# Optimization experiments

Hardware: AMD Instinct MI355X
Metric: run time of the kernel (lower is better)

Reference implementation:

```python
import jax, jax.numpy as jnp
import numpy as np

TWO_PI = 2.0 * np.pi
ROTATION_PROB = 0.5


def _rodrigues(axis, angle):
    """Vectorized Rodrigues formula. axis: [G,3] (unnormalized), angle: [G] in [0,1) (scaled by 2pi).
    Returns R: [G,3,3]."""
    ax = axis / jnp.linalg.norm(axis, axis=-1, keepdims=True)
    a0, a1, a2 = ax[:, 0], ax[:, 1], ax[:, 2]
    z = jnp.zeros_like(a0)
    # Skew-symmetric cross-product matrix K per graph: [G,3,3]
    K = jnp.stack([
        jnp.stack([z, -a2, a1], axis=-1),
        jnp.stack([a2, z, -a0], axis=-1),
        jnp.stack([-a1, a0, z], axis=-1),
    ], axis=-2)
    theta = (angle * TWO_PI)[:, None, None]
    I = jnp.eye(3, dtype=axis.dtype)
    return I + jnp.sin(theta) * K + (1.0 - jnp.cos(theta)) * jnp.matmul(K, K)


def setup_inputs() -> dict:
    key = jax.random.key(0)
    ks = jax.random.split(key, 8)
    G, N, E = 8192, 2_000_000, 16_000_000
    x = jax.random.normal(ks[0], (N, 3), dtype=jnp.float32)
    edge_attr = jax.random.normal(ks[1], (E, 3), dtype=jnp.float32)
    y = jax.random.normal(ks[2], (G, 3), dtype=jnp.float32)
    node_batch = jnp.sort(jax.random.randint(ks[3], (N,), 0, G, dtype=jnp.int32))
    edge_batch = jnp.sort(jax.random.randint(ks[4], (E,), 0, G, dtype=jnp.int32))
    axis = jax.random.normal(ks[5], (G, 3), dtype=jnp.float32)
    angle = jax.random.uniform(ks[6], (G,), dtype=jnp.float32)
    apply_rand = jax.random.uniform(ks[7], (G,), dtype=jnp.float32)
    return {"x": x, "edge_attr": edge_attr, "y": y, "node_batch": node_batch,
            "edge_batch": edge_batch, "axis": axis, "angle": angle,
            "apply_rand": apply_rand}


def reference(x, edge_attr, y, node_batch, edge_batch, axis, angle, apply_rand):
    R = _rodrigues(axis, angle)  # [G,3,3]
    I = jnp.eye(3, dtype=x.dtype)
    # Only rotate graphs where the coin flip succeeds (identity otherwise)
    R = jnp.where((apply_rand < ROTATION_PROB)[:, None, None], R, I)
    # v @ R.T  ==  out[n,j] = sum_i v[n,i] * R[j,i]
    x_out = jnp.einsum('ni,nji->nj', x, R[node_batch])
    e_out = jnp.einsum('ei,eji->ej', edge_attr, R[edge_batch])
    y_out = jnp.einsum('gi,gji->gj', y, R)
    return x_out, e_out, y_out
```

## Files before the change

### kernel.cpp

```cpp
#include <hip/hip_runtime.h>
#include <math.h>

#define TWO_PI_F 6.283185307179586f
#define ROWS 1024
#define BLK  256

typedef float f32x4 __attribute__((ext_vector_type(4)));

__global__ void compute_R_kernel(const float* __restrict__ axis,
                                 const float* __restrict__ angle,
                                 const float* __restrict__ apply_rand,
                                 float* __restrict__ R, int G) {
    int g = blockIdx.x * blockDim.x + threadIdx.x;
    if (g >= G) return;
    float a = axis[3 * g + 0];
    float b = axis[3 * g + 1];
    float c = axis[3 * g + 2];
    float inv = rsqrtf(a * a + b * b + c * c);
    a *= inv; b *= inv; c *= inv;
    float th = angle[g] * TWO_PI_F;
    float s, co;
    sincosf(th, &s, &co);
    float omc = 1.0f - co;

    float r00 = 1.0f - omc * (b * b + c * c);
    float r01 = -s * c + omc * (a * b);
    float r02 =  s * b + omc * (a * c);
    float r10 =  s * c + omc * (a * b);
    float r11 = 1.0f - omc * (a * a + c * c);
    float r12 = -s * a + omc * (b * c);
    float r20 = -s * b + omc * (a * c);
    float r21 =  s * a + omc * (b * c);
    float r22 = 1.0f - omc * (a * a + b * b);

    if (!(apply_rand[g] < 0.5f)) {
        r00 = 1.0f; r01 = 0.0f; r02 = 0.0f;
        r10 = 0.0f; r11 = 1.0f; r12 = 0.0f;
        r20 = 0.0f; r21 = 0.0f; r22 = 1.0f;
    }
    float4* Rg = reinterpret_cast<float4*>(R + 12 * (size_t)g);
    Rg[0] = make_float4(r00, r01, r02, 0.0f);
    Rg[1] = make_float4(r10, r11, r12, 0.0f);
    Rg[2] = make_float4(r20, r21, r22, 0.0f);
}

template <bool HAS_BATCH>
__global__ __launch_bounds__(BLK) void apply_rot_lds(
        const float* __restrict__ v,
        const int* __restrict__ batch,
        const float* __restrict__ R,
        float* __restrict__ out, int n) {
    __shared__ float buf[ROWS * 3];
    float4* buf4 = reinterpret_cast<float4*>(buf);

    const int tid = threadIdx.x;
    const size_t rowBase = (size_t)blockIdx.x * ROWS;
    int rows = n - (int)rowBase;
    if (rows > ROWS) rows = ROWS;
    const int floatsHere = rows * 3;
    const int f4Here = floatsHere >> 2;
    const int tailFloats = floatsHere & 3;
    const int nRow4 = rows >> 2;

    int4 bi = make_int4(0, 0, 0, 0);
    if (tid < nRow4) {
        if (HAS_BATCH) {
            bi = *(reinterpret_cast<const int4*>(batch + rowBase) + tid);
        } else {
            int base = (int)rowBase + 4 * tid;
            bi = make_int4(base, base + 1, base + 2, base + 3);
        }
    }

    {
        const float4* src = reinterpret_cast<const float4*>(v + rowBase * 3);
        if (tid < f4Here)       buf4[tid]       = src[tid];
        if (tid + 256 < f4Here) buf4[tid + 256] = src[tid + 256];
        if (tid + 512 < f4Here) buf4[tid + 512] = src[tid + 512];
        if (tailFloats && tid < tailFloats) {
            int fi = (f4Here << 2) + tid;
            buf[fi] = v[rowBase * 3 + fi];
        }
    }
    __syncthreads();

    if (tid < nRow4) {
        float4 p0 = buf4[3 * tid + 0];
        float4 p1 = buf4[3 * tid + 1];
        float4 p2 = buf4[3 * tid + 2];
        float rowsv[4][3] = {
            {p0.x, p0.y, p0.z},
            {p0.w, p1.x, p1.y},
            {p1.z, p1.w, p2.x},
            {p2.y, p2.z, p2.w}};
        int gs[4] = {bi.x, bi.y, bi.z, bi.w};
        float oo[12];
#pragma unroll
        for (int r = 0; r < 4; ++r) {
            const float4* Rg = reinterpret_cast<const float4*>(R + 12 * (size_t)gs[r]);
            float4 R0 = Rg[0];
            float4 R1 = Rg[1];
            float4 R2 = Rg[2];
            float v0 = rowsv[r][0], v1 = rowsv[r][1], v2 = rowsv[r][2];
            oo[3 * r + 0] = R0.x * v0 + R0.y * v1 + R0.z * v2;
            oo[3 * r + 1] = R1.x * v0 + R1.y * v1 + R1.z * v2;
            oo[3 * r + 2] = R2.x * v0 + R2.y * v1 + R2.z * v2;
        }
        buf4[3 * tid + 0] = make_float4(oo[0], oo[1], oo[2], oo[3]);
        buf4[3 * tid + 1] = make_float4(oo[4], oo[5], oo[6], oo[7]);
        buf4[3 * tid + 2] = make_float4(oo[8], oo[9], oo[10], oo[11]);
    } else if (tid == nRow4 && (rows & 3)) {
        for (int r = nRow4 * 4; r < rows; ++r) {
            size_t row = rowBase + r;
            int g = HAS_BATCH ? batch[row] : (int)row;
            const float* Rg = R + 12 * (size_t)g;
            float v0 = buf[3 * r + 0], v1 = buf[3 * r + 1], v2 = buf[3 * r + 2];
            float t0 = Rg[0] * v0 + Rg[1] * v1 + Rg[2]  * v2;
            float t1 = Rg[4] * v0 + Rg[5] * v1 + Rg[6]  * v2;
            float t2 = Rg[8] * v0 + Rg[9] * v1 + Rg[10] * v2;
            buf[3 * r + 0] = t0; buf[3 * r + 1] = t1; buf[3 * r + 2] = t2;
        }
    }
    __syncthreads();

    {
        const f32x4* b4 = reinterpret_cast<const f32x4*>(buf);
        f32x4* dst = reinterpret_cast<f32x4*>(out + rowBase * 3);
        if (tid < f4Here) {
            f32x4 val = b4[tid];
            __builtin_nontemporal_store(val, &dst[tid]);
        }
        if (tid + 256 < f4Here) {
            f32x4 val = b4[tid + 256];
            __builtin_nontemporal_store(val, &dst[tid + 256]);
        }
        if (tid + 512 < f4Here) {
            f32x4 val = b4[tid + 512];
            __builtin_nontemporal_store(val, &dst[tid + 512]);
        }
        if (tailFloats && tid < tailFloats) {
            int fi = (f4Here << 2) + tid;
            __builtin_nontemporal_store(buf[fi], &out[rowBase * 3 + fi]);
        }
    }
}

extern "C" void kernel_launch(void* const* d_in, const int* in_sizes, int n_in,
                              void* d_out, int out_size, void* d_ws, size_t ws_size,
                              hipStream_t stream) {
    const float* x          = (const float*)d_in[0];
    const float* edge_attr  = (const float*)d_in[1];
    const float* y          = (const float*)d_in[2];
    const int*   node_batch = (const int*)d_in[3];
    const int*   edge_batch = (const int*)d_in[4];
    const float* axis       = (const float*)d_in[5];
    const float* angle      = (const float*)d_in[6];
    const float* apply_rand = (const float*)d_in[7];

    const int N = in_sizes[3];
    const int E = in_sizes[4];
    const int G = in_sizes[6];

    float* R = (float*)d_ws;
    float* x_out = (float*)d_out;
    float* e_out = x_out + 3 * (size_t)N;
    float* y_out = e_out + 3 * (size_t)E;

    compute_R_kernel<<<(G + BLK - 1) / BLK, BLK, 0, stream>>>(
        axis, angle, apply_rand, R, G);

    int nbN = (N + ROWS - 1) / ROWS;
    int nbE = (E + ROWS - 1) / ROWS;
    int nbG = (G + ROWS - 1) / ROWS;

    apply_rot_lds<true><<<nbE, BLK, 0, stream>>>(edge_attr, edge_batch, R, e_out, E);
    apply_rot_lds<true><<<nbN, BLK, 0, stream>>>(x, node_batch, R, x_out, N);
    apply_rot_lds<false><<<nbG, BLK, 0, stream>>>(y, nullptr, R, y_out, G);
}
```

Baseline: 102.3 us.

## Process two tiles per block with register prefetch of the second tile

Each block now handles two 1024-row tiles. Both tiles' input and batch loads are issued up front into registers. The first tile is then rotated and stored while the second tile's data is still arriving, so more global loads are in flight per thread. This doubles LDS use per block (24 KB) and raises register pressure, which can lower occupancy, and it adds extra barriers.

```diff
diff --git a/kernel.cpp b/kernel.cpp
--- a/kernel.cpp
+++ b/kernel.cpp
@@ -45,45 +45,12 @@
 }
 
 template <bool HAS_BATCH>
-__global__ __launch_bounds__(BLK) void apply_rot_lds(
-        const float* __restrict__ v,
-        const int* __restrict__ batch,
-        const float* __restrict__ R,
-        float* __restrict__ out, int n) {
-    __shared__ float buf[ROWS * 3];
-    float4* buf4 = reinterpret_cast<float4*>(buf);
-
-    const int tid = threadIdx.x;
-    const size_t rowBase = (size_t)blockIdx.x * ROWS;
-    int rows = n - (int)rowBase;
-    if (rows > ROWS) rows = ROWS;
-    const int floatsHere = rows * 3;
-    const int f4Here = floatsHere >> 2;
-    const int tailFloats = floatsHere & 3;
+__device__ __forceinline__ void rotate_tile(float* bufLds, int4 bi,
+                                            const float* __restrict__ R,
+                                            const int* __restrict__ batch,
+                                            size_t rowBase, int rows, int tid) {
+    float4* buf4 = reinterpret_cast<float4*>(bufLds);
     const int nRow4 = rows >> 2;
-
-    int4 bi = make_int4(0, 0, 0, 0);
-    if (tid < nRow4) {
-        if (HAS_BATCH) {
-            bi = *(reinterpret_cast<const int4*>(batch + rowBase) + tid);
-        } else {
-            int base = (int)rowBase + 4 * tid;
-            bi = make_int4(base, base + 1, base + 2, base + 3);
-        }
-    }
-
-    {
-        const float4* src = reinterpret_cast<const float4*>(v + rowBase * 3);
-        if (tid < f4Here)       buf4[tid]       = src[tid];
-        if (tid + 256 < f4Here) buf4[tid + 256] = src[tid + 256];
-        if (tid + 512 < f4Here) buf4[tid + 512] = src[tid + 512];
-        if (tailFloats && tid < tailFloats) {
-            int fi = (f4Here << 2) + tid;
-            buf[fi] = v[rowBase * 3 + fi];
-        }
-    }
-    __syncthreads();
-
     if (tid < nRow4) {
         float4 p0 = buf4[3 * tid + 0];
         float4 p1 = buf4[3 * tid + 1];
@@ -114,34 +81,116 @@
             size_t row = rowBase + r;
             int g = HAS_BATCH ? batch[row] : (int)row;
             const float* Rg = R + 12 * (size_t)g;
-            float v0 = buf[3 * r + 0], v1 = buf[3 * r + 1], v2 = buf[3 * r + 2];
+            float v0 = bufLds[3 * r + 0], v1 = bufLds[3 * r + 1], v2 = bufLds[3 * r + 2];
             float t0 = Rg[0] * v0 + Rg[1] * v1 + Rg[2]  * v2;
             float t1 = Rg[4] * v0 + Rg[5] * v1 + Rg[6]  * v2;
             float t2 = Rg[8] * v0 + Rg[9] * v1 + Rg[10] * v2;
-            buf[3 * r + 0] = t0; buf[3 * r + 1] = t1; buf[3 * r + 2] = t2;
+            bufLds[3 * r + 0] = t0; bufLds[3 * r + 1] = t1; bufLds[3 * r + 2] = t2;
         }
     }
+}
+
+__device__ __forceinline__ void store_tile_nt(const float* bufLds,
+                                              float* __restrict__ out,
+                                              size_t rowBase, int rows, int tid) {
+    const int floatsHere = rows * 3;
+    const int f4Here = floatsHere >> 2;
+    const int tailFloats = floatsHere & 3;
+    const f32x4* b4 = reinterpret_cast<const f32x4*>(bufLds);
+    f32x4* dst = reinterpret_cast<f32x4*>(out + rowBase * 3);
+    if (tid < f4Here) {
+        f32x4 val = b4[tid];
+        __builtin_nontemporal_store(val, &dst[tid]);
+    }
+    if (tid + 256 < f4Here) {
+        f32x4 val = b4[tid + 256];
+        __builtin_nontemporal_store(val, &dst[tid + 256]);
+    }
+    if (tid + 512 < f4Here) {
+        f32x4 val = b4[tid + 512];
+        __builtin_nontemporal_store(val, &dst[tid + 512]);
+    }
+    if (tailFloats && tid < tailFloats) {
+        int fi = (f4Here << 2) + tid;
+        __builtin_nontemporal_store(bufLds[fi], &out[rowBase * 3 + fi]);
+    }
+}
+
+template <bool HAS_BATCH>
+__global__ __launch_bounds__(BLK) void apply_rot_lds2(
+        const float* __restrict__ v,
+        const int* __restrict__ batch,
+        const float* __restrict__ R,
+        float* __restrict__ out, int n) {
+    __shared__ float buf[2][ROWS * 3];
+    const int tid = threadIdx.x;
+
+    size_t rb0 = (size_t)(blockIdx.x * 2) * ROWS;
+    size_t rb1 = rb0 + ROWS;
+    int rows0 = n - (int)rb0; rows0 = rows0 < 0 ? 0 : (rows0 > ROWS ? ROWS : rows0);
+    int rows1 = n - (int)rb1; rows1 = rows1 < 0 ? 0 : (rows1 > ROWS ? ROWS : rows1);
+
+    float4 p00 = make_float4(0, 0, 0, 0), p01 = p00, p02 = p00;
+    float4 p10 = p00, p11 = p00, p12 = p00;
+    float t0f = 0.f, t1f = 0.f;
+    int4 bi0 = make_int4(0, 0, 0, 0), bi1 = bi0;
+    {
+        const float4* src0 = reinterpret_cast<const float4*>(v + rb0 * 3);
+        int f40 = (rows0 * 3) >> 2;
+        if (tid < f40)       p00 = src0[tid];
+        if (tid + 256 < f40) p01 = src0[tid + 256];
+        if (tid + 512 < f40) p02 = src0[tid + 512];
+        int tf0 = (rows0 * 3) & 3;
+        if (tf0 && tid < tf0) t0f = v[rb0 * 3 + (((size_t)f40) << 2) + tid];
+    }
+    if (rows1 > 0) {
+        const float4* src1 = reinterpret_cast<const float4*>(v + rb1 * 3);
+        int f41 = (rows1 * 3) >> 2;
+        if (tid < f41)       p10 = src1[tid];
+        if (tid + 256 < f41) p11 = src1[tid + 256];
+        if (tid + 512 < f41) p12 = src1[tid + 512];
+        int tf1 = (rows1 * 3) & 3;
+        if (tf1 && tid < tf1) t1f = v[rb1 * 3 + (((size_t)f41) << 2) + tid];
+    }
+    if (tid < (rows0 >> 2)) {
+        if (HAS_BATCH) bi0 = *(reinterpret_cast<const int4*>(batch + rb0) + tid);
+        else { int b = (int)rb0 + 4 * tid; bi0 = make_int4(b, b + 1, b + 2, b + 3); }
+    }
+    if (rows1 > 0 && tid < (rows1 >> 2)) {
+        if (HAS_BATCH) bi1 = *(reinterpret_cast<const int4*>(batch + rb1) + tid);
+        else { int b = (int)rb1 + 4 * tid; bi1 = make_int4(b, b + 1, b + 2, b + 3); }
+    }
+
+    {
+        float4* b4 = reinterpret_cast<float4*>(buf[0]);
+        int f40 = (rows0 * 3) >> 2;
+        if (tid < f40)       b4[tid]       = p00;
+        if (tid + 256 < f40) b4[tid + 256] = p01;
+        if (tid + 512 < f40) b4[tid + 512] = p02;
+        int tf0 = (rows0 * 3) & 3;
+        if (tf0 && tid < tf0) buf[0][(f40 << 2) + tid] = t0f;
+    }
     __syncthreads();
 
-    {
-        const f32x4* b4 = reinterpret_cast<const f32x4*>(buf);
-        f32x4* dst = reinterpret_cast<f32x4*>(out + rowBase * 3);
-        if (tid < f4Here) {
-            f32x4 val = b4[tid];
-            __builtin_nontemporal_store(val, &dst[tid]);
-        }
-        if (tid + 256 < f4Here) {
-            f32x4 val = b4[tid + 256];
-            __builtin_nontemporal_store(val, &dst[tid + 256]);
-        }
-        if (tid + 512 < f4Here) {
-            f32x4 val = b4[tid + 512];
-            __builtin_nontemporal_store(val, &dst[tid + 512]);
-        }
-        if (tailFloats && tid < tailFloats) {
-            int fi = (f4Here << 2) + tid;
-            __builtin_nontemporal_store(buf[fi], &out[rowBase * 3 + fi]);
-        }
+    rotate_tile<HAS_BATCH>(buf[0], bi0, R, batch, rb0, rows0, tid);
+    __syncthreads();
+
+    if (rows1 > 0) {
+        float4* b4 = reinterpret_cast<float4*>(buf[1]);
+        int f41 = (rows1 * 3) >> 2;
+        if (tid < f41)       b4[tid]       = p10;
+        if (tid + 256 < f41) b4[tid + 256] = p11;
+        if (tid + 512 < f41) b4[tid + 512] = p12;
+        int tf1 = (rows1 * 3) & 3;
+        if (tf1 && tid < tf1) buf[1][(f41 << 2) + tid] = t1f;
+    }
+    store_tile_nt(buf[0], out, rb0, rows0, tid);
+
+    if (rows1 > 0) {
+        __syncthreads();
+        rotate_tile<HAS_BATCH>(buf[1], bi1, R, batch, rb1, rows1, tid);
+        __syncthreads();
+        store_tile_nt(buf[1], out, rb1, rows1, tid);
     }
 }
 
@@ -169,11 +218,11 @@
     compute_R_kernel<<<(G + BLK - 1) / BLK, BLK, 0, stream>>>(
         axis, angle, apply_rand, R, G);
 
-    int nbN = (N + ROWS - 1) / ROWS;
-    int nbE = (E + ROWS - 1) / ROWS;
-    int nbG = (G + ROWS - 1) / ROWS;
-
-    apply_rot_lds<true><<<nbE, BLK, 0, stream>>>(edge_attr, edge_batch, R, e_out, E);
-    apply_rot_lds<true><<<nbN, BLK, 0, stream>>>(x, node_batch, R, x_out, N);
-    apply_rot_lds<false><<<nbG, BLK, 0, stream>>>(y, nullptr, R, y_out, G);
-}
+    int nbE = (int)(((size_t)E + 2 * ROWS - 1) / (2 * ROWS));
+    int nbN = (int)(((size_t)N + 2 * ROWS - 1) / (2 * ROWS));
+    int nbG = (int)(((size_t)G + 2 * ROWS - 1) / (2 * ROWS));
+
+    apply_rot_lds2<true><<<nbE, BLK, 0, stream>>>(edge_attr, edge_batch, R, e_out, E);
+    apply_rot_lds2<true><<<nbN, BLK, 0, stream>>>(x, node_batch, R, x_out, N);
+    apply_rot_lds2<false><<<nbG, BLK, 0, stream>>>(y, nullptr, R, y_out, G);
+}
```

After: 101.4 us. About the same (-0.9%).
